# Kernel tuning notes

Measured on AMD Instinct MI355X. Metric: run time of the kernel, lower is better.

## Reference

```python
import jax, jax.numpy as jnp
import numpy as np

N = 4096
D_MODEL = 512


def setup_inputs() -> dict:
    key = jax.random.key(0)
    ks = jax.random.split(key, 5)
    scale = 1.0 / np.sqrt(D_MODEL)
    return {
        "x": jax.random.normal(ks[0], (N, D_MODEL), dtype=jnp.float32),
        "Wq": jax.random.normal(ks[1], (D_MODEL, D_MODEL), dtype=jnp.float32) * scale,
        "Wk": jax.random.normal(ks[2], (D_MODEL, D_MODEL), dtype=jnp.float32) * scale,
        "Wv": jax.random.normal(ks[3], (D_MODEL, D_MODEL), dtype=jnp.float32) * scale,
        "Ws": jax.random.normal(ks[4], (1, D_MODEL), dtype=jnp.float32) * scale,
    }


def reference(x, Wq, Wk, Wv, Ws):
    # x: [N, d]; torch nn.Linear(bias=False) computes x @ W.T
    Q = x @ Wq.T  # [N, d]
    K = x @ Wk.T  # [N, d]
    V = x @ Wv.T  # [N, d]
    sigma = jnp.clip(x @ Ws.T, 0.001, 1.0)  # [N, 1]

    # prior association: Gaussian kernel over |i - j| with per-row sigma
    pos = jnp.arange(sigma.shape[0], dtype=jnp.float32)
    diff = jnp.abs(pos[:, None] - pos[None, :])  # [N, N]
    gaussian = jnp.exp(-0.5 * (diff / sigma) ** 2) / jnp.sqrt(2.0 * jnp.pi * sigma)
    P = gaussian / (gaussian.sum(axis=1, keepdims=True) + 1e-8)

    scale = jnp.sqrt(jnp.float32(x.shape[-1]))
    S = jax.nn.softmax((Q @ K.T) / scale, axis=-1)  # [N, N]
    Z = S @ V  # [N, d]
    return Z, P, S
```

## Files before the change

### kernel.cpp

```cpp
#include <hip/hip_runtime.h>
#include <math.h>

#define N_TOK 4096
#define DM 512

typedef _Float16 f16x8 __attribute__((ext_vector_type(8)));
typedef _Float16 f16x4 __attribute__((ext_vector_type(4)));
typedef float f32x4 __attribute__((ext_vector_type(4)));

__device__ __forceinline__ void async_ld16(const ushort* g, ushort* l) {
  __builtin_amdgcn_global_load_lds(
      (const __attribute__((address_space(1))) void*)g,
      (__attribute__((address_space(3))) void*)l, 16, 0, 0);
}

template <int N>
__device__ __forceinline__ void vm_wait() {
  asm volatile("s_waitcnt vmcnt(%0)" ::"i"(N) : "memory");
}

__global__ __launch_bounds__(256) void pack_sigma(
    const float* __restrict__ x, const float* __restrict__ Wq,
    const float* __restrict__ Wk, const float* __restrict__ Wv,
    const float* __restrict__ Ws, _Float16* __restrict__ x16,
    _Float16* __restrict__ Wc16, float* __restrict__ sg) {
  const int b = blockIdx.x;
  const int t = threadIdx.x;
  if (b < 2048) {
    int i = b * 1024 + t * 4;
    float4 v = *(const float4*)&x[i];
    f16x4 o;
    o.x = (_Float16)v.x; o.y = (_Float16)v.y;
    o.z = (_Float16)v.z; o.w = (_Float16)v.w;
    *(f16x4*)&x16[i] = o;
    int col = (t * 4) & 511;
    float4 w = *(const float4*)&Ws[col];
    float p = v.x * w.x + v.y * w.y + v.z * w.z + v.w * w.w;
    __shared__ float red[256];
    red[t] = p;
    __syncthreads();
    int lt = t & 127;
    for (int off = 64; off > 0; off >>= 1) {
      if (lt < off) red[t] += red[t + off];
      __syncthreads();
    }
    if (lt == 0) {
      float s = red[t];
      sg[2 * b + (t >> 7)] = fminf(fmaxf(s, 0.001f), 1.0f);
    }
  } else {
    int e = (b - 2048) * 1024 + t * 4;
    const float* src;
    int le = e & (DM * DM - 1);
    if (e < DM * DM) src = Wq + le;
    else if (e < 2 * DM * DM) src = Wk + le;
    else src = Wv + le;
    float4 v = *(const float4*)src;
    f16x4 o;
    o.x = (_Float16)v.x; o.y = (_Float16)v.y;
    o.z = (_Float16)v.z; o.w = (_Float16)v.w;
    *(f16x4*)&Wc16[e] = o;
  }
}

template <int BM, int BN, int BK, int NT, int EPI>
__global__ __launch_bounds__(256) void gemm_pipe(
    const _Float16* __restrict__ A, int lda, const _Float16* __restrict__ B,
    int ldb, float scale, _Float16* __restrict__ D0,
    _Float16* __restrict__ D1, _Float16* __restrict__ D2,
    float2* __restrict__ Part) {
  constexpr int TB = (BM + BN) * BK;
  constexpr int ACH = BM * BK / 8;
  constexpr int BCH = BN * BK / 8;
  constexpr int L = (ACH + BCH) / 256;
  constexpr int MI = BM / 32;
  constexpr int NJ = BN / 32;
  __shared__ _Float16 lds[3 * TB];
  const int t = threadIdx.x;

  const int w = t >> 6, Ln = t & 63;
  const int wm = (w >> 1) * (BM / 2), wn = (w & 1) * (BN / 2);
  const int row = Ln & 15, quad = Ln >> 4;
  const int bm = blockIdx.y * BM, bn = blockIdx.x * BN;

  f32x4 acc[MI][NJ] = {{}};

  const ushort* gp[L];
#pragma unroll
  for (int k = 0; k < L; ++k) {
    int c = t + k * 256;
    if (c < ACH) {
      int r = c / (BK / 8), c8 = c % (BK / 8);
      gp[k] = (const ushort*)(A + (size_t)(bm + r) * lda + c8 * 8);
    } else {
      int cb = c - ACH;
      int r = cb / (BK / 8), c8 = cb % (BK / 8);
      gp[k] = (const ushort*)(B + (size_t)(bn + r) * ldb + c8 * 8);
    }
  }

  auto stage = [&](int buf) {
    _Float16* dst = lds + buf * TB;
#pragma unroll
    for (int k = 0; k < L; ++k) {
      async_ld16(gp[k], (ushort*)(dst + (t + k * 256) * 8));
      gp[k] += BK;
    }
  };

  stage(0);
  stage(1);

  for (int tt = 0; tt < NT; ++tt) {
    const int cur = tt % 3;
    if (tt + 2 < NT) stage((tt + 2) % 3);
    if (tt < NT - 2) vm_wait<2 * L>();
    else if (tt == NT - 2) vm_wait<L>();
    else vm_wait<0>();
    __builtin_amdgcn_s_barrier();

    const _Float16* Ah = lds + cur * TB;
    const _Float16* Bh = Ah + BM * BK;
    f16x8 af[BK / 32][MI], bf[BK / 32][NJ];
#pragma unroll
    for (int kk = 0; kk < BK / 32; ++kk) {
#pragma unroll
      for (int i = 0; i < MI; ++i)
        af[kk][i] =
            *(const f16x8*)&Ah[(wm + i * 16 + row) * BK + kk * 32 + quad * 8];
#pragma unroll
      for (int j = 0; j < NJ; ++j)
        bf[kk][j] =
            *(const f16x8*)&Bh[(wn + j * 16 + row) * BK + kk * 32 + quad * 8];
    }
#pragma unroll
    for (int kk = 0; kk < BK / 32; ++kk)
#pragma unroll
      for (int i = 0; i < MI; ++i)
#pragma unroll
        for (int j = 0; j < NJ; ++j)
          acc[i][j] = __builtin_amdgcn_mfma_f32_16x16x32_f16(
              af[kk][i], bf[kk][j], acc[i][j], 0, 0, 0);

    asm volatile("s_waitcnt lgkmcnt(0)" ::: "memory");
    __builtin_amdgcn_s_barrier();
  }

  if constexpr (EPI == 1) {
    const int region = bn >> 9;
    if (region < 2) {
      _Float16* D = (region == 0) ? D0 : D1;
#pragma unroll
      for (int i = 0; i < MI; ++i)
#pragma unroll
        for (int j = 0; j < NJ; ++j)
#pragma unroll
          for (int r = 0; r < 4; ++r) {
            int gr = bm + wm + i * 16 + quad * 4 + r;
            int nn = (bn & 511) + wn + j * 16 + row;
            D[(size_t)gr * 512 + nn] = (_Float16)acc[i][j][r];
          }
    } else {
      _Float16* T = lds;
#pragma unroll
      for (int i = 0; i < MI; ++i)
#pragma unroll
        for (int j = 0; j < NJ; ++j) {
          int nn = wn + j * 16 + row;
          int gr0 = wm + i * 16 + quad * 4;
          f16x4 v;
          v.x = (_Float16)acc[i][j][0]; v.y = (_Float16)acc[i][j][1];
          v.z = (_Float16)acc[i][j][2]; v.w = (_Float16)acc[i][j][3];
          *(f16x4*)&T[nn * 136 + gr0] = v;
        }
      __syncthreads();
#pragma unroll
      for (int c = 0; c < 8; ++c) {
        int cc = t + c * 256;
        int nn = cc >> 4;
        int g8 = (cc & 15) * 8;
        f16x8 v = *(const f16x8*)&T[nn * 136 + g8];
        *(f16x8*)&D2[(size_t)((bn & 511) + nn) * 4096 + bm + g8] = v;
      }
    }
  } else {
    float2* Ml = (float2*)lds;
#pragma unroll
    for (int i = 0; i < MI; ++i)
#pragma unroll
      for (int r = 0; r < 4; ++r) {
        float sv[NJ];
        int gr = bm + wm + i * 16 + quad * 4 + r;
#pragma unroll
        for (int j = 0; j < NJ; ++j) {
          _Float16 h = (_Float16)(acc[i][j][r] * scale);
          D0[(size_t)gr * N_TOK + bn + wn + j * 16 + row] = h;
          sv[j] = (float)h;
        }
        float m = sv[0];
#pragma unroll
        for (int j = 1; j < NJ; ++j) m = fmaxf(m, sv[j]);
#pragma unroll
        for (int off = 1; off < 16; off <<= 1)
          m = fmaxf(m, __shfl_xor(m, off));
        float se = 0.f;
#pragma unroll
        for (int j = 0; j < NJ; ++j) se += __expf(sv[j] - m);
#pragma unroll
        for (int off = 1; off < 16; off <<= 1) se += __shfl_xor(se, off);
        if (row == 0) {
          int rb = wm + i * 16 + quad * 4 + r;
          Ml[(w & 1) * BM + rb] = make_float2(m, se);
        }
      }
    __syncthreads();
    {
      float2 a = Ml[t];
      float2 b2 = Ml[BM + t];
      float m = fmaxf(a.x, b2.x);
      float l = a.y * __expf(a.x - m) + b2.y * __expf(b2.x - m);
      Part[(size_t)(bm + t) * 32 + blockIdx.x] = make_float2(m, l);
    }
  }
}

template <int WITH_P>
__global__ __launch_bounds__(256) void sv_fused(
    const _Float16* __restrict__ Sc, const float2* __restrict__ stats,
    const _Float16* __restrict__ VT, float* __restrict__ Z,
    float* __restrict__ S, const float* __restrict__ sigma,
    float* __restrict__ P) {
  constexpr int BM = 64, BN = 128, BK = 64, NT = N_TOK / BK;
  constexpr int TB = (BM + BN) * BK;
  constexpr int ACH = BM * BK / 8;
  constexpr int L = (ACH + BN * BK / 8) / 256;
  __shared__ _Float16 lds[3 * TB];
  const int t = threadIdx.x;
  const int b = blockIdx.x;

  if (WITH_P && b >= 512) {
    float* red = (float*)lds;
    const int pidx = b - 512;
    const int wv = t >> 6, lane = t & 63;
#pragma unroll 1
    for (int rr = 0; rr < 4; ++rr) {
      const int i = pidx * 4 + rr;
      const float sgv = sigma[i];
      const float inv2 = -0.5f / (sgv * sgv);
      const float cc = rsqrtf(6.283185307179586f * sgv);
      float4 g[4];
      float sum = 0.f;
#pragma unroll
      for (int r = 0; r < 4; ++r) {
        int j = r * 1024 + t * 4;
        float d0 = (float)(i - j);
        float d1 = d0 - 1.f, d2 = d0 - 2.f, d3 = d0 - 3.f;
        g[r].x = __expf(inv2 * d0 * d0) * cc;
        g[r].y = __expf(inv2 * d1 * d1) * cc;
        g[r].z = __expf(inv2 * d2 * d2) * cc;
        g[r].w = __expf(inv2 * d3 * d3) * cc;
        sum += g[r].x + g[r].y + g[r].z + g[r].w;
      }
#pragma unroll
      for (int off = 32; off > 0; off >>= 1) sum += __shfl_xor(sum, off);
      if (lane == 0) red[wv] = sum;
      __syncthreads();
      const float inv = 1.0f / (red[0] + red[1] + red[2] + red[3] + 1e-8f);
      float* Prow = P + (size_t)i * N_TOK;
#pragma unroll
      for (int r = 0; r < 4; ++r) {
        g[r].x *= inv; g[r].y *= inv; g[r].z *= inv; g[r].w *= inv;
        *(float4*)&Prow[r * 1024 + t * 4] = g[r];
      }
      __syncthreads();
    }
    return;
  }

  if (b >= 256) {
    const int rs = (b - 256) * 16;
    float2* pm = (float2*)lds;
    float* sm = (float*)(pm + 256);
    float* si = sm + 16;
    {
      int rr = t >> 4, kh = t & 15;
      float2 p0 = stats[(size_t)(rs + rr) * 32 + 2 * kh];
      float2 p1 = stats[(size_t)(rs + rr) * 32 + 2 * kh + 1];
      float m = fmaxf(p0.x, p1.x);
      float l = p0.y * __expf(p0.x - m) + p1.y * __expf(p1.x - m);
      pm[t] = make_float2(m, l);
    }
    __syncthreads();
    if (t < 16) {
      float m = -INFINITY, l = 0.f;
#pragma unroll
      for (int k = 0; k < 16; ++k) {
        float2 pr = pm[t * 16 + k];
        float nm = fmaxf(m, pr.x);
        l = l * __expf(m - nm) + pr.y * __expf(pr.x - nm);
        m = nm;
      }
      sm[t] = m;
      si[t] = 1.0f / l;
    }
    __syncthreads();
#pragma unroll 1
    for (int r = 0; r < 16; ++r) {
      const int rowg = rs + r;
      const float m = sm[r], linv = si[r];
      const _Float16* src = Sc + (size_t)rowg * N_TOK + t * 16;
      float* dst = S + (size_t)rowg * N_TOK + t * 16;
      f16x8 h0 = *(const f16x8*)src;
      f16x8 h1 = *(const f16x8*)(src + 8);
      float4 o0, o1, o2, o3;
      o0.x = __expf((float)h0[0] - m) * linv;
      o0.y = __expf((float)h0[1] - m) * linv;
      o0.z = __expf((float)h0[2] - m) * linv;
      o0.w = __expf((float)h0[3] - m) * linv;
      o1.x = __expf((float)h0[4] - m) * linv;
      o1.y = __expf((float)h0[5] - m) * linv;
      o1.z = __expf((float)h0[6] - m) * linv;
      o1.w = __expf((float)h0[7] - m) * linv;
      o2.x = __expf((float)h1[0] - m) * linv;
      o2.y = __expf((float)h1[1] - m) * linv;
      o2.z = __expf((float)h1[2] - m) * linv;
      o2.w = __expf((float)h1[3] - m) * linv;
      o3.x = __expf((float)h1[4] - m) * linv;
      o3.y = __expf((float)h1[5] - m) * linv;
      o3.z = __expf((float)h1[6] - m) * linv;
      o3.w = __expf((float)h1[7] - m) * linv;
      *(float4*)(dst + 0) = o0;
      *(float4*)(dst + 4) = o1;
      *(float4*)(dst + 8) = o2;
      *(float4*)(dst + 12) = o3;
    }
    return;
  }

  const int w = t >> 6, Ln = t & 63;
  const int wm = (w >> 1) * 32, wn = (w & 1) * 64;
  const int row = Ln & 15, quad = Ln >> 4;
  const int bm = (b >> 2) * BM, bn = (b & 3) * BN;

  float mrow[2], linv[2];
#pragma unroll
  for (int i = 0; i < 2; ++i) {
    const int gr = bm + wm + i * 16 + row;
    float m = -INFINITY, l = 0.f;
#pragma unroll
    for (int kb = 0; kb < 32; ++kb) {
      float2 pr = stats[(size_t)gr * 32 + kb];
      float nm = fmaxf(m, pr.x);
      l = l * __expf(m - nm) + pr.y * __expf(pr.x - nm);
      m = nm;
    }
    mrow[i] = m;
    linv[i] = 1.0f / l;
  }

  f32x4 acc[2][4] = {{}};

  const ushort* gp[L];
#pragma unroll
  for (int k = 0; k < L; ++k) {
    int c = t + k * 256;
    if (c < ACH) {
      int r = c >> 3, c8 = c & 7;
      gp[k] = (const ushort*)(Sc + (size_t)(bm + r) * N_TOK + c8 * 8);
    } else {
      int cb = c - ACH;
      int r = cb >> 3, c8 = cb & 7;
      gp[k] = (const ushort*)(VT + (size_t)(bn + r) * N_TOK + c8 * 8);
    }
  }
  auto stage = [&](int buf) {
    _Float16* dst = lds + buf * TB;
#pragma unroll
    for (int k = 0; k < L; ++k) {
      async_ld16(gp[k], (ushort*)(dst + (t + k * 256) * 8));
      gp[k] += BK;
    }
  };

  stage(0);
  stage(1);

  for (int tt = 0; tt < NT; ++tt) {
    const int cur = tt % 3;
    if (tt + 2 < NT) stage((tt + 2) % 3);
    if (tt < NT - 2) vm_wait<2 * L>();
    else if (tt == NT - 2) vm_wait<L>();
    else vm_wait<0>();
    __builtin_amdgcn_s_barrier();

    const _Float16* Ah = lds + cur * TB;
    const _Float16* Bh = Ah + BM * BK;
    f16x8 af[2][2], bf[2][4];
#pragma unroll
    for (int kk = 0; kk < 2; ++kk) {
#pragma unroll
      for (int i = 0; i < 2; ++i) {
        f16x8 raw = *(const f16x8*)&Ah[(wm + i * 16 + row) * BK + kk * 32 +
                                       quad * 8];
        f16x8 pa;
#pragma unroll
        for (int e = 0; e < 8; ++e)
          pa[e] = (_Float16)(__expf((float)raw[e] - mrow[i]) * linv[i]);
        af[kk][i] = pa;
      }
#pragma unroll
      for (int j = 0; j < 4; ++j)
        bf[kk][j] =
            *(const f16x8*)&Bh[(wn + j * 16 + row) * BK + kk * 32 + quad * 8];
    }
#pragma unroll
    for (int kk = 0; kk < 2; ++kk)
#pragma unroll
      for (int i = 0; i < 2; ++i)
#pragma unroll
        for (int j = 0; j < 4; ++j)
          acc[i][j] = __builtin_amdgcn_mfma_f32_16x16x32_f16(
              af[kk][i], bf[kk][j], acc[i][j], 0, 0, 0);

    asm volatile("s_waitcnt lgkmcnt(0)" ::: "memory");
    __builtin_amdgcn_s_barrier();
  }

#pragma unroll
  for (int i = 0; i < 2; ++i)
#pragma unroll
    for (int j = 0; j < 4; ++j)
#pragma unroll
      for (int r = 0; r < 4; ++r) {
        int gr = bm + wm + i * 16 + quad * 4 + r;
        int gc = bn + wn + j * 16 + row;
        Z[(size_t)gr * DM + gc] = acc[i][j][r];
      }
}

__global__ __launch_bounds__(256) void tailP(const float* __restrict__ sigma,
                                             float* __restrict__ P) {
  __shared__ float red[256];
  const int t = threadIdx.x;
  const int i = blockIdx.x;
  const float sg = sigma[i];
  const float inv2 = -0.5f / (sg * sg);
  const float c = rsqrtf(6.283185307179586f * sg);
  float4 g[4];
  float sum = 0.f;
#pragma unroll
  for (int r = 0; r < 4; ++r) {
    int j = r * 1024 + t * 4;
    float d0 = (float)(i - j);
    float d1 = d0 - 1.f, d2 = d0 - 2.f, d3 = d0 - 3.f;
    g[r].x = __expf(inv2 * d0 * d0) * c;
    g[r].y = __expf(inv2 * d1 * d1) * c;
    g[r].z = __expf(inv2 * d2 * d2) * c;
    g[r].w = __expf(inv2 * d3 * d3) * c;
    sum += g[r].x + g[r].y + g[r].z + g[r].w;
  }
  red[t] = sum;
  __syncthreads();
  for (int off = 128; off > 0; off >>= 1) {
    if (t < off) red[t] += red[t + off];
    __syncthreads();
  }
  const float inv = 1.0f / (red[0] + 1e-8f);
  float* Prow = P + (size_t)i * N_TOK;
#pragma unroll
  for (int r = 0; r < 4; ++r) {
    g[r].x *= inv; g[r].y *= inv; g[r].z *= inv; g[r].w *= inv;
    *(float4*)&Prow[r * 1024 + t * 4] = g[r];
  }
}

extern "C" void kernel_launch(void* const* d_in, const int* in_sizes, int n_in,
                              void* d_out, int out_size, void* d_ws,
                              size_t ws_size, hipStream_t stream) {
  const float* x = (const float*)d_in[0];
  const float* Wq = (const float*)d_in[1];
  const float* Wk = (const float*)d_in[2];
  const float* Wv = (const float*)d_in[3];
  const float* Ws = (const float*)d_in[4];

  float* out = (float*)d_out;
  float* Z = out;
  float* Pout = Z + (size_t)N_TOK * DM;
  float* S = Pout + (size_t)N_TOK * N_TOK;

  const size_t E = (size_t)N_TOK * DM;

  _Float16* x16 = (_Float16*)d_ws;
  _Float16* Wc16 = x16 + E;
  float* sg = (float*)(Wc16 + 3 * DM * DM);
  float2* pstats = (float2*)(sg + 4096);
  _Float16* stage = (_Float16*)(pstats + (size_t)N_TOK * 32);

  const size_t stage_bytes = (3 * E + (size_t)N_TOK * N_TOK) * sizeof(_Float16);
  const size_t base_bytes = (size_t)((char*)stage - (char*)d_ws);
  const bool ws_ok = ws_size >= base_bytes + stage_bytes;

  _Float16* Q16 = ws_ok ? stage : (_Float16*)Pout;
  _Float16* K16 = Q16 + E;
  _Float16* VT16 = K16 + E;
  _Float16* Sc16 = VT16 + E;

  const dim3 blk(256);
  const float qk_scale = 1.0f / sqrtf((float)DM);

  pack_sigma<<<2816, blk, 0, stream>>>(x, Wq, Wk, Wv, Ws, x16, Wc16, sg);

  gemm_pipe<128, 128, 32, 16, 1><<<dim3(12, 32), blk, 0, stream>>>(
      x16, DM, Wc16, DM, 1.0f, Q16, K16, VT16, nullptr);

  gemm_pipe<256, 128, 32, 16, 3><<<dim3(32, 16), blk, 0, stream>>>(
      Q16, DM, K16, DM, qk_scale, Sc16, nullptr, nullptr, pstats);

  if (ws_ok) {
    sv_fused<1><<<dim3(1536), blk, 0, stream>>>(Sc16, pstats, VT16, Z, S, sg,
                                                Pout);
  } else {
    sv_fused<0><<<dim3(512), blk, 0, stream>>>(Sc16, pstats, VT16, Z, S,
                                               nullptr, nullptr);
    tailP<<<N_TOK, blk, 0, stream>>>(sg, Pout);
  }
}
```

Before: 274.9 us.

## Split softmax normalization from SV GEMM and write normalized probabilities back in place

The fused kernel, which recomputed exp on the A tiles inside the SV GEMM and ran S normalization in separate blocks, is split into two launches. A normalize kernel with one block per row writes S as fp32 and also overwrites the fp16 score buffer with normalized probabilities. A plain GEMM then multiplies them with V^T. The LDS layout changes to two 32-wide k halves. This removes the redundant exp work from the GEMM inner loop but adds an extra fp16 write and read of the N×N matrix, an extra launch, and the loss of overlap between the P/S blocks and the GEMM blocks.

```diff
diff --git a/kernel.cpp b/kernel.cpp
--- a/kernel.cpp
+++ b/kernel.cpp
@@ -225,22 +225,16 @@
 }
 
 template <int WITH_P>
-__global__ __launch_bounds__(256) void sv_fused(
-    const _Float16* __restrict__ Sc, const float2* __restrict__ stats,
-    const _Float16* __restrict__ VT, float* __restrict__ Z,
+__global__ __launch_bounds__(256) void normalize_kernel(
+    const float2* __restrict__ stats, _Float16* __restrict__ Sc,
     float* __restrict__ S, const float* __restrict__ sigma,
     float* __restrict__ P) {
-  constexpr int BM = 64, BN = 128, BK = 64, NT = N_TOK / BK;
-  constexpr int TB = (BM + BN) * BK;
-  constexpr int ACH = BM * BK / 8;
-  constexpr int L = (ACH + BN * BK / 8) / 256;
-  __shared__ _Float16 lds[3 * TB];
   const int t = threadIdx.x;
   const int b = blockIdx.x;
 
-  if (WITH_P && b >= 512) {
-    float* red = (float*)lds;
-    const int pidx = b - 512;
+  if (WITH_P && b >= N_TOK) {
+    __shared__ float red[4];
+    const int pidx = b - N_TOK;
     const int wv = t >> 6, lane = t & 63;
 #pragma unroll 1
     for (int rr = 0; rr < 4; ++rr) {
@@ -277,109 +271,72 @@
     return;
   }
 
-  if (b >= 256) {
-    const int rs = (b - 256) * 16;
-    float2* pm = (float2*)lds;
-    float* sm = (float*)(pm + 256);
-    float* si = sm + 16;
-    {
-      int rr = t >> 4, kh = t & 15;
-      float2 p0 = stats[(size_t)(rs + rr) * 32 + 2 * kh];
-      float2 p1 = stats[(size_t)(rs + rr) * 32 + 2 * kh + 1];
-      float m = fmaxf(p0.x, p1.x);
-      float l = p0.y * __expf(p0.x - m) + p1.y * __expf(p1.x - m);
-      pm[t] = make_float2(m, l);
-    }
-    __syncthreads();
-    if (t < 16) {
-      float m = -INFINITY, l = 0.f;
-#pragma unroll
-      for (int k = 0; k < 16; ++k) {
-        float2 pr = pm[t * 16 + k];
-        float nm = fmaxf(m, pr.x);
-        l = l * __expf(m - nm) + pr.y * __expf(pr.x - nm);
-        m = nm;
-      }
-      sm[t] = m;
-      si[t] = 1.0f / l;
-    }
-    __syncthreads();
-#pragma unroll 1
-    for (int r = 0; r < 16; ++r) {
-      const int rowg = rs + r;
-      const float m = sm[r], linv = si[r];
-      const _Float16* src = Sc + (size_t)rowg * N_TOK + t * 16;
-      float* dst = S + (size_t)rowg * N_TOK + t * 16;
-      f16x8 h0 = *(const f16x8*)src;
-      f16x8 h1 = *(const f16x8*)(src + 8);
-      float4 o0, o1, o2, o3;
-      o0.x = __expf((float)h0[0] - m) * linv;
-      o0.y = __expf((float)h0[1] - m) * linv;
-      o0.z = __expf((float)h0[2] - m) * linv;
-      o0.w = __expf((float)h0[3] - m) * linv;
-      o1.x = __expf((float)h0[4] - m) * linv;
-      o1.y = __expf((float)h0[5] - m) * linv;
-      o1.z = __expf((float)h0[6] - m) * linv;
-      o1.w = __expf((float)h0[7] - m) * linv;
-      o2.x = __expf((float)h1[0] - m) * linv;
-      o2.y = __expf((float)h1[1] - m) * linv;
-      o2.z = __expf((float)h1[2] - m) * linv;
-      o2.w = __expf((float)h1[3] - m) * linv;
-      o3.x = __expf((float)h1[4] - m) * linv;
-      o3.y = __expf((float)h1[5] - m) * linv;
-      o3.z = __expf((float)h1[6] - m) * linv;
-      o3.w = __expf((float)h1[7] - m) * linv;
-      *(float4*)(dst + 0) = o0;
-      *(float4*)(dst + 4) = o1;
-      *(float4*)(dst + 8) = o2;
-      *(float4*)(dst + 12) = o3;
-    }
-    return;
-  }
-
+  float2 pr = stats[(size_t)b * 32 + (t & 31)];
+  float m = pr.x, l = pr.y;
+#pragma unroll
+  for (int off = 1; off < 32; off <<= 1) {
+    float mo = __shfl_xor(m, off);
+    float lo = __shfl_xor(l, off);
+    float nm = fmaxf(m, mo);
+    l = l * __expf(m - nm) + lo * __expf(mo - nm);
+    m = nm;
+  }
+  const float linv = 1.0f / l;
+
+  _Float16* src = Sc + (size_t)b * N_TOK + t * 16;
+  float* dst = S + (size_t)b * N_TOK + t * 16;
+  f16x8 h0 = *(const f16x8*)src;
+  f16x8 h1 = *(const f16x8*)(src + 8);
+  float e[16];
+#pragma unroll
+  for (int k = 0; k < 8; ++k) e[k] = __expf((float)h0[k] - m) * linv;
+#pragma unroll
+  for (int k = 0; k < 8; ++k) e[8 + k] = __expf((float)h1[k] - m) * linv;
+#pragma unroll
+  for (int q = 0; q < 4; ++q) {
+    float4 o;
+    o.x = e[q * 4]; o.y = e[q * 4 + 1]; o.z = e[q * 4 + 2]; o.w = e[q * 4 + 3];
+    *(float4*)(dst + q * 4) = o;
+  }
+  f16x8 p0, p1;
+#pragma unroll
+  for (int k = 0; k < 8; ++k) {
+    p0[k] = (_Float16)e[k];
+    p1[k] = (_Float16)e[8 + k];
+  }
+  *(f16x8*)src = p0;
+  *(f16x8*)(src + 8) = p1;
+}
+
+__global__ __launch_bounds__(256) void sv_gemm(const _Float16* __restrict__ A,
+                                               const _Float16* __restrict__ B,
+                                               float* __restrict__ Z) {
+  constexpr int BK = 64, NT = N_TOK / BK;
+  constexpr int TB = (64 + 128) * BK;
+  __shared__ _Float16 lds[3 * TB];
+  const int t = threadIdx.x;
   const int w = t >> 6, Ln = t & 63;
   const int wm = (w >> 1) * 32, wn = (w & 1) * 64;
   const int row = Ln & 15, quad = Ln >> 4;
-  const int bm = (b >> 2) * BM, bn = (b & 3) * BN;
-
-  float mrow[2], linv[2];
-#pragma unroll
-  for (int i = 0; i < 2; ++i) {
-    const int gr = bm + wm + i * 16 + row;
-    float m = -INFINITY, l = 0.f;
-#pragma unroll
-    for (int kb = 0; kb < 32; ++kb) {
-      float2 pr = stats[(size_t)gr * 32 + kb];
-      float nm = fmaxf(m, pr.x);
-      l = l * __expf(m - nm) + pr.y * __expf(pr.x - nm);
-      m = nm;
-    }
-    mrow[i] = m;
-    linv[i] = 1.0f / l;
-  }
+  const int bm = (blockIdx.x >> 2) * 64, bn = (blockIdx.x & 3) * 128;
 
   f32x4 acc[2][4] = {{}};
 
-  const ushort* gp[L];
-#pragma unroll
-  for (int k = 0; k < L; ++k) {
-    int c = t + k * 256;
-    if (c < ACH) {
-      int r = c >> 3, c8 = c & 7;
-      gp[k] = (const ushort*)(Sc + (size_t)(bm + r) * N_TOK + c8 * 8);
-    } else {
-      int cb = c - ACH;
-      int r = cb >> 3, c8 = cb & 7;
-      gp[k] = (const ushort*)(VT + (size_t)(bn + r) * N_TOK + c8 * 8);
-    }
-  }
+  const int rA = t >> 2, oA = (t & 3) * 8;
+  const ushort* ga = (const ushort*)(A + (size_t)(bm + rA) * N_TOK + oA);
+  const ushort* gb0 = (const ushort*)(B + (size_t)(bn + rA) * N_TOK + oA);
+  const ushort* gb1 = (const ushort*)(B + (size_t)(bn + rA + 64) * N_TOK + oA);
+
   auto stage = [&](int buf) {
-    _Float16* dst = lds + buf * TB;
-#pragma unroll
-    for (int k = 0; k < L; ++k) {
-      async_ld16(gp[k], (ushort*)(dst + (t + k * 256) * 8));
-      gp[k] += BK;
-    }
+    _Float16* Ah = lds + buf * TB;
+    _Float16* Bh = Ah + 64 * BK;
+    async_ld16(ga, (ushort*)(Ah + t * 8));
+    async_ld16(ga + 32, (ushort*)(Ah + 2048 + t * 8));
+    async_ld16(gb0, (ushort*)(Bh + t * 8));
+    async_ld16(gb1, (ushort*)(Bh + (t + 256) * 8));
+    async_ld16(gb0 + 32, (ushort*)(Bh + 4096 + t * 8));
+    async_ld16(gb1 + 32, (ushort*)(Bh + 4096 + (t + 256) * 8));
+    ga += 64; gb0 += 64; gb1 += 64;
   };
 
   stage(0);
@@ -388,30 +345,24 @@
   for (int tt = 0; tt < NT; ++tt) {
     const int cur = tt % 3;
     if (tt + 2 < NT) stage((tt + 2) % 3);
-    if (tt < NT - 2) vm_wait<2 * L>();
-    else if (tt == NT - 2) vm_wait<L>();
+    if (tt < NT - 2) vm_wait<12>();
+    else if (tt == NT - 2) vm_wait<6>();
     else vm_wait<0>();
     __builtin_amdgcn_s_barrier();
 
     const _Float16* Ah = lds + cur * TB;
-    const _Float16* Bh = Ah + BM * BK;
+    const _Float16* Bh = Ah + 64 * BK;
     f16x8 af[2][2], bf[2][4];
 #pragma unroll
     for (int kk = 0; kk < 2; ++kk) {
 #pragma unroll
-      for (int i = 0; i < 2; ++i) {
-        f16x8 raw = *(const f16x8*)&Ah[(wm + i * 16 + row) * BK + kk * 32 +
-                                       quad * 8];
-        f16x8 pa;
-#pragma unroll
-        for (int e = 0; e < 8; ++e)
-          pa[e] = (_Float16)(__expf((float)raw[e] - mrow[i]) * linv[i]);
-        af[kk][i] = pa;
-      }
+      for (int i = 0; i < 2; ++i)
+        af[kk][i] =
+            *(const f16x8*)&Ah[kk * 2048 + (wm + i * 16 + row) * 32 + quad * 8];
 #pragma unroll
       for (int j = 0; j < 4; ++j)
         bf[kk][j] =
-            *(const f16x8*)&Bh[(wn + j * 16 + row) * BK + kk * 32 + quad * 8];
+            *(const f16x8*)&Bh[kk * 4096 + (wn + j * 16 + row) * 32 + quad * 8];
     }
 #pragma unroll
     for (int kk = 0; kk < 2; ++kk)
@@ -517,11 +468,13 @@
       Q16, DM, K16, DM, qk_scale, Sc16, nullptr, nullptr, pstats);
 
   if (ws_ok) {
-    sv_fused<1><<<dim3(1536), blk, 0, stream>>>(Sc16, pstats, VT16, Z, S, sg,
-                                                Pout);
+    normalize_kernel<1><<<dim3(4096 + 1024), blk, 0, stream>>>(pstats, Sc16, S,
+                                                               sg, Pout);
+    sv_gemm<<<dim3(256), blk, 0, stream>>>(Sc16, VT16, Z);
   } else {
-    sv_fused<0><<<dim3(512), blk, 0, stream>>>(Sc16, pstats, VT16, Z, S,
-                                               nullptr, nullptr);
+    normalize_kernel<0><<<dim3(4096), blk, 0, stream>>>(pstats, Sc16, S,
+                                                        nullptr, nullptr);
+    sv_gemm<<<dim3(256), blk, 0, stream>>>(Sc16, VT16, Z);
     tailP<<<N_TOK, blk, 0, stream>>>(sg, Pout);
   }
 }
```

After: 272.3 us. Within noise of the previous version (-0.9%).
